# Kernel optimization log

Measured on AMD Instinct MI355X. Metric: run time of the kernel, lower is better.

Reference implementation:

```python
import jax, jax.numpy as jnp
import numpy as np

B, C, H, W = 4, 512, 64, 64


def setup_inputs() -> dict:
    key = jax.random.key(0)
    ks = jax.random.split(key, 9)
    s = 0.02
    return {
        "x": jax.random.normal(ks[0], (B, C, H, W), dtype=jnp.float32),
        "Wq": jax.random.normal(ks[1], (C, C), dtype=jnp.float32) * s,
        "bq": jnp.zeros((C,), dtype=jnp.float32),
        "Wk": jax.random.normal(ks[2], (C, C), dtype=jnp.float32) * s,
        "bk": jnp.zeros((C,), dtype=jnp.float32),
        "Wv": jax.random.normal(ks[3], (C, C), dtype=jnp.float32) * s,
        "bv": jnp.zeros((C,), dtype=jnp.float32),
        "Wo": jax.random.normal(ks[4], (C, C), dtype=jnp.float32) * s,
        "bo": jnp.zeros((C,), dtype=jnp.float32),
    }


def reference(x, Wq, bq, Wk, bk, Wv, bv, Wo, bo):
    b, c, h, w = x.shape
    # (b, c, h, w) -> (b, N, c) flattened spatial tokens
    t = jnp.swapaxes(x.reshape(b, c, h * w), 1, 2)
    q = t @ Wq.T + bq
    k = t @ Wk.T + bk
    v = t @ Wv.T + bv
    scale = 1.0 / jnp.sqrt(jnp.asarray(c, dtype=t.dtype))
    scores = jnp.einsum("bnc,bmc->bnm", q, k) * scale  # (b, N, N)
    attn = jax.nn.softmax(scores, axis=-1)
    out = jnp.einsum("bnm,bmc->bnc", attn, v)
    out = out @ Wo.T + bo  # dropout p=0.0 is identity
    # Faithful to original: direct view (b,N,c) -> (b,c,h,w) WITHOUT permute
    return out.reshape(b, c, h, w)
```

## Files before the change

### kernel.cpp

```cpp
#include <hip/hip_runtime.h>


#define B_ 4
#define C_ 512
#define N_ 4096
#define KV_ 32
#define NSTEP 128

typedef unsigned short u16;
typedef __attribute__((ext_vector_type(8))) short bf16x8;
typedef __attribute__((ext_vector_type(4))) float f32x4;

#define MFMA16(a,b,c) __builtin_amdgcn_mfma_f32_16x16x32_bf16((a),(b),(c),0,0,0)

__device__ inline float exp2_fast(float x){
#if __has_builtin(__builtin_amdgcn_exp2f)
  return __builtin_amdgcn_exp2f(x);
#else
  return exp2f(x);
#endif
}

__device__ inline u16 f2bf(float f){
  unsigned u = __float_as_uint(f);
  u += 0x7FFFu + ((u >> 16) & 1u);
  return (u16)(u >> 16);
}

__device__ __forceinline__ void gload16(const char* g, char* l){
#if __has_builtin(__builtin_amdgcn_global_load_lds)
  __builtin_amdgcn_global_load_lds(
      (const __attribute__((address_space(1))) unsigned int*)(unsigned long long)g,
      (__attribute__((address_space(3))) unsigned int*)(unsigned int)(unsigned long long)l,
      16, 0, 0);
#else
  int lane = threadIdx.x & 63;
  *(uint4*)(l + lane*16) = *(const uint4*)g;
#endif
}

__global__ __launch_bounds__(256) void conv_w_kernel(const float* wq, const float* wk,
                                                     const float* wv, const float* wo, u16* out){
  int i = (blockIdx.x * 256 + threadIdx.x) * 8;
  int mat = i >> 18;
  int within = i & 262143;
  const float* s = (mat==0) ? wq : (mat==1) ? wk : (mat==2) ? wv : wo;
  float4 a = *(const float4*)(s + within);
  float4 b = *(const float4*)(s + within + 4);
  unsigned u0 = f2bf(a.x) | ((unsigned)f2bf(a.y) << 16);
  unsigned u1 = f2bf(a.z) | ((unsigned)f2bf(a.w) << 16);
  unsigned u2 = f2bf(b.x) | ((unsigned)f2bf(b.y) << 16);
  unsigned u3 = f2bf(b.z) | ((unsigned)f2bf(b.w) << 16);
  uint4 v = {u0,u1,u2,u3};
  *(uint4*)(out + i) = v;
}

__global__ __launch_bounds__(256) void transpose_kernel(const float* x, u16* T){
  __shared__ u16 tile[64][66];
  int b = blockIdx.z; int n0 = blockIdx.x*64; int c0 = blockIdx.y*64;
  int t = threadIdx.x;
  const float* xb = x + (size_t)b*C_*N_;
  int nn = t & 63, r0 = t >> 6;
  #pragma unroll
  for (int i=0;i<16;i++){
    int r = r0 + i*4;
    tile[r][nn] = f2bf(xb[(size_t)(c0+r)*N_ + n0 + nn]);
  }
  __syncthreads();
  int nrow = t >> 2, cs = t & 3;
  unsigned u[8];
  #pragma unroll
  for (int j=0;j<8;j++){
    u16 lo = tile[cs*16 + 2*j    ][nrow];
    u16 hi = tile[cs*16 + 2*j + 1][nrow];
    u[j] = lo | ((unsigned)hi << 16);
  }
  u16* dst = T + (size_t)b*N_*C_ + (size_t)(n0+nrow)*C_ + c0 + cs*16;
  uint4 v0 = {u[0],u[1],u[2],u[3]};
  uint4 v1 = {u[4],u[5],u[6],u[7]};
  *(uint4*)(dst)     = v0;
  *(uint4*)(dst + 8) = v1;
}

template<int MODE>
__global__ __launch_bounds__(256) void proj_kernel(const u16* Abase, const u16* Wb,
                                                   const float* b0, const float* b1, const float* b2,
                                                   u16* Qo, u16* Ko, u16* VTo, float* Fo){
  __shared__ char lds[32768];
  char* Al = lds;
  char* Bl = lds + 16384;
  int z = blockIdx.z;
  int b, mat;
  if constexpr (MODE==0){ b = z/3; mat = z - b*3; } else { b = z; mat = 3; }
  const u16* A = Abase + (size_t)b*N_*C_;
  const u16* W = Wb + (size_t)mat*C_*C_;
  const float* bias = (MODE==0) ? (mat==0?b0:(mat==1?b1:b2)) : b0;
  int n0 = blockIdx.x*128, c0 = blockIdx.y*128;
  int t = threadIdx.x, lane = t & 63, w = t >> 6;
  int wm = w >> 1, wn = w & 1;
  int l15 = lane & 15, l4 = lane >> 4;
  f32x4 acc[4][4];
  #pragma unroll
  for (int i=0;i<4;i++)
    #pragma unroll
    for (int j=0;j<4;j++) acc[i][j] = f32x4{0.f,0.f,0.f,0.f};

  for (int ks=0; ks<8; ks++){
    int k0 = ks*64;
    __syncthreads();
    #pragma unroll
    for (int it=0; it<4; it++){
      int idx = it*256 + t, row = idx>>3, ch = idx&7;
      uint4 v = *(const uint4*)(A + (size_t)(n0+row)*C_ + k0 + ch*8);
      *(uint4*)(Al + row*128 + ((ch*16) ^ ((row&7)<<4))) = v;
    }
    #pragma unroll
    for (int it=0; it<4; it++){
      int idx = it*256 + t, row = idx>>3, ch = idx&7;
      uint4 v = *(const uint4*)(W + (size_t)(c0+row)*C_ + k0 + ch*8);
      *(uint4*)(Bl + row*128 + ((ch*16) ^ ((row&7)<<4))) = v;
    }
    __syncthreads();
    #pragma unroll
    for (int kk=0; kk<2; kk++){
      bf16x8 bfrag[4];
      #pragma unroll
      for (int ni=0; ni<4; ni++){
        int br = wn*64 + ni*16 + l15;
        bfrag[ni] = *(const bf16x8*)(Bl + br*128 + ((kk*64 + l4*16) ^ ((br&7)<<4)));
      }
      #pragma unroll
      for (int mi=0; mi<4; mi++){
        int ar = wm*64 + mi*16 + l15;
        bf16x8 afrag = *(const bf16x8*)(Al + ar*128 + ((kk*64 + l4*16) ^ ((ar&7)<<4)));
        #pragma unroll
        for (int ni=0; ni<4; ni++) acc[mi][ni] = MFMA16(afrag, bfrag[ni], acc[mi][ni]);
      }
    }
  }
  #pragma unroll
  for (int mi=0; mi<4; mi++){
    #pragma unroll
    for (int ni=0; ni<4; ni++){
      int col  = c0 + wn*64 + ni*16 + l15;
      int rowb = n0 + wm*64 + mi*16 + l4*4;
      float bb = bias[col];
      if constexpr (MODE==1){
        #pragma unroll
        for (int r=0;r<4;r++)
          Fo[(size_t)b*N_*C_ + (size_t)(rowb+r)*C_ + col] = acc[mi][ni][r] + bb;
      } else {
        if (mat==0){
          #pragma unroll
          for (int r=0;r<4;r++)
            Qo[(size_t)b*N_*C_ + (size_t)(rowb+r)*C_ + col] = f2bf(acc[mi][ni][r] + bb);
        } else if (mat==1){
          #pragma unroll
          for (int r=0;r<4;r++)
            Ko[(size_t)b*N_*C_ + (size_t)(rowb+r)*C_ + col] = f2bf(acc[mi][ni][r] + bb);
        } else {
          ushort4 pk;
          pk.x = f2bf(acc[mi][ni][0] + bb);
          pk.y = f2bf(acc[mi][ni][1] + bb);
          pk.z = f2bf(acc[mi][ni][2] + bb);
          pk.w = f2bf(acc[mi][ni][3] + bb);
          *(ushort4*)(VTo + (size_t)b*(size_t)C_*N_ + (size_t)col*N_ + rowb) = pk;
        }
      }
    }
  }
}

__global__ __launch_bounds__(512) __attribute__((amdgpu_waves_per_eu(2, 2)))
void attn_kernel(const u16* Q, const u16* K, const u16* VT, u16* O){
  extern __shared__ char sm[];
  char* Pl   = sm + 131072;
  float* fac  = (float*)(sm + 135168);
  float* lrow = (float*)(sm + 135424);
  const float SC = (float)(1.4426950408889634 / 22.627416997969522);

  int t = threadIdx.x, lane = t & 63, w = t >> 6;
  int l15 = lane & 15, l4 = lane >> 4;
  int d = blockIdx.x;
  int L = (d & 7)*32 + (d >> 3);
  int b = L >> 6, qt = L & 63;
  int n0 = qt*64;

  const char* Kg = (const char*)K  + (size_t)b*N_*C_*2;
  const char* Vg = (const char*)VT + (size_t)b*C_*N_*2;

  auto stage = [&](int step, int sel){
    int kv0 = step*KV_;
    char* Kn = sm + sel*32768;
    char* Vn = sm + 65536 + sel*32768;
    #pragma unroll
    for (int i=0;i<4;i++){
      int row = w*4 + i;
      gload16(Kg + (size_t)(kv0+row)*1024 + ((lane*16) ^ ((row&7)<<4)), Kn + row*1024);
    }
    int rr = lane >> 2, bb = (lane & 3)*16;
    #pragma unroll
    for (int i=0;i<4;i++){
      int c = w*4 + i;
      gload16(Vg + (size_t)(c*16+rr)*8192 + (size_t)kv0*2 + (bb ^ ((rr&3)<<4)), Vn + c*1024);
    }
  };

  bf16x8 qf[16];
  if (w < 4){
    const u16* qp = Q + ((size_t)b*N_ + n0 + 16*w + l15)*C_ + l4*8;
    #pragma unroll
    for (int kc=0;kc<16;kc++) qf[kc] = *(const bf16x8*)(qp + kc*32);
  }

  f32x4 acc[4][4];
  #pragma unroll
  for (int i=0;i<4;i++)
    #pragma unroll
    for (int j=0;j<4;j++) acc[i][j] = f32x4{0.f,0.f,0.f,0.f};
  float m[4], lsum[4];
  #pragma unroll
  for (int r=0;r<4;r++){ m[r] = -1e30f; lsum[r] = 0.f; }

  stage(0, 0);
  __syncthreads();

  for (int s=0; s<NSTEP; s++){
    char* Kc = sm + (s&1)*32768;
    char* Vc = sm + 65536 + (s&1)*32768;
    if (s+1 < NSTEP) stage(s+1, (s+1)&1);

    if (w < 4){
      f32x4 sa[2];
      sa[0] = f32x4{0.f,0.f,0.f,0.f}; sa[1] = f32x4{0.f,0.f,0.f,0.f};
      #pragma unroll
      for (int kc=0;kc<16;kc++){
        #pragma unroll
        for (int sub=0;sub<2;sub++){
          int kr = sub*16 + l15;
          bf16x8 kf = *(const bf16x8*)(Kc + kr*1024 + ((kc*64 + l4*16) ^ ((kr&7)<<4)));
          sa[sub] = MFMA16(qf[kc], kf, sa[sub]);
        }
      }
      float uu[2][4], pmax[4];
      #pragma unroll
      for (int r=0;r<4;r++){
        float x0 = sa[0][r]*SC, x1 = sa[1][r]*SC;
        uu[0][r]=x0; uu[1][r]=x1;
        pmax[r] = fmaxf(x0,x1);
      }
      #pragma unroll
      for (int off=1; off<16; off<<=1){
        #pragma unroll
        for (int r=0;r<4;r++) pmax[r] = fmaxf(pmax[r], __shfl_xor(pmax[r], off));
      }
      bool need = false;
      #pragma unroll
      for (int r=0;r<4;r++) need = need || (pmax[r] > m[r] + 11.5f);
      float fv[4];
      if (__any(need)){
        #pragma unroll
        for (int r=0;r<4;r++){
          float mn = fmaxf(m[r], pmax[r]);
          fv[r] = exp2_fast(m[r]-mn);
          m[r] = mn; lsum[r] *= fv[r];
        }
      } else {
        #pragma unroll
        for (int r=0;r<4;r++) fv[r] = 1.0f;
      }
      if (l15 == 0){
        #pragma unroll
        for (int r=0;r<4;r++) fac[16*w + l4*4 + r] = fv[r];
      }
      float rs[4] = {0.f,0.f,0.f,0.f};
      #pragma unroll
      for (int sub=0;sub<2;sub++){
        #pragma unroll
        for (int r=0;r<4;r++){
          float p = exp2_fast(uu[sub][r] - m[r]);
          rs[r] += p;
          int row = 16*w + l4*4 + r, col = sub*16 + l15;
          *(u16*)(Pl + row*64 + ((col*2) ^ ((row&3)<<4))) = f2bf(p);
        }
      }
      #pragma unroll
      for (int off=1; off<16; off<<=1){
        #pragma unroll
        for (int r=0;r<4;r++) rs[r] += __shfl_xor(rs[r], off);
      }
      #pragma unroll
      for (int r=0;r<4;r++) lsum[r] += rs[r];
    }
    __syncthreads();

    f32x4 facv[4];
    #pragma unroll
    for (int mi=0;mi<4;mi++) facv[mi] = *(const f32x4*)(fac + mi*16 + l4*4);
    #pragma unroll
    for (int mi=0;mi<4;mi++)
      #pragma unroll
      for (int ni=0;ni<4;ni++)
        #pragma unroll
        for (int r=0;r<4;r++) acc[mi][ni][r] *= facv[mi][r];

    bf16x8 vf[4];
    #pragma unroll
    for (int ni=0;ni<4;ni++){
      int crow = w*64 + ni*16 + l15;
      vf[ni] = *(const bf16x8*)(Vc + crow*64 + ((l4*16) ^ ((crow&3)<<4)));
    }
    #pragma unroll
    for (int mi=0;mi<4;mi++){
      int prow = mi*16 + l15;
      bf16x8 pa = *(const bf16x8*)(Pl + prow*64 + ((l4*16) ^ ((prow&3)<<4)));
      #pragma unroll
      for (int ni=0;ni<4;ni++) acc[mi][ni] = MFMA16(pa, vf[ni], acc[mi][ni]);
    }
    __syncthreads();
  }

  if (w < 4 && l15 == 0){
    #pragma unroll
    for (int r=0;r<4;r++) lrow[16*w + l4*4 + r] = lsum[r];
  }
  __syncthreads();
  u16* Ob = O + ((size_t)b*N_ + n0)*C_;
  #pragma unroll
  for (int mi=0;mi<4;mi++){
    f32x4 lv = *(const f32x4*)(lrow + mi*16 + l4*4);
    f32x4 rl;
    #pragma unroll
    for (int r=0;r<4;r++) rl[r] = 1.0f / lv[r];
    #pragma unroll
    for (int ni=0;ni<4;ni++){
      #pragma unroll
      for (int r=0;r<4;r++){
        int row = mi*16 + l4*4 + r, col = w*64 + ni*16 + l15;
        Ob[(size_t)row*C_ + col] = f2bf(acc[mi][ni][r]*rl[r]);
      }
    }
  }
}

extern "C" void kernel_launch(void* const* d_in, const int* in_sizes, int n_in,
                              void* d_out, int out_size, void* d_ws, size_t ws_size,
                              hipStream_t stream){
  const float* x  = (const float*)d_in[0];
  const float* Wq = (const float*)d_in[1];
  const float* bq = (const float*)d_in[2];
  const float* Wk = (const float*)d_in[3];
  const float* bk = (const float*)d_in[4];
  const float* Wv = (const float*)d_in[5];
  const float* bv = (const float*)d_in[6];
  const float* Wo = (const float*)d_in[7];
  const float* bo = (const float*)d_in[8];

  char* ws = (char*)d_ws;
  u16* Tb  = (u16*)(ws);
  u16* Wbf = (u16*)(ws + 16777216);
  u16* Qw  = (u16*)(ws + 18874368);
  u16* Kw  = (u16*)(ws + 35651584);
  u16* VTw = (u16*)(ws + 52428800);

  hipFuncSetAttribute((const void*)attn_kernel, hipFuncAttributeMaxDynamicSharedMemorySize, 135680);

  conv_w_kernel<<<512,256,0,stream>>>(Wq,Wk,Wv,Wo,Wbf);
  transpose_kernel<<<dim3(64,8,4),256,0,stream>>>(x, Tb);
  proj_kernel<0><<<dim3(32,4,12),256,0,stream>>>(Tb, Wbf, bq,bk,bv, Qw,Kw,VTw,nullptr);
  attn_kernel<<<dim3(256),512,135680,stream>>>(Qw,Kw,VTw,Tb);
  proj_kernel<1><<<dim3(32,4,4),256,0,stream>>>(Tb, Wbf, bo,nullptr,nullptr, nullptr,nullptr,nullptr,(float*)d_out);
}
```

Measured before the change: 444.3 us.

## Split QK^T and softmax across all eight waves with cross-wave max/sum exchange

The score computation and softmax were done by only 4 of the 8 waves while the others idled. Now every wave computes one 16-column half of the KV tile, and the two halves share row maxima and row sums through small LDS buffers. A per-step flag lets waves skip the accumulator rescale when no wave raised its running max. The plain barriers are replaced with explicit waitcnt plus s_barrier helpers, and the P tile swizzle is changed. The cost is an extra barrier per step and a little more LDS, which could hurt if sync latency dominates.

```diff
diff --git a/kernel.cpp b/kernel.cpp
--- a/kernel.cpp
+++ b/kernel.cpp
@@ -25,6 +25,19 @@
   unsigned u = __float_as_uint(f);
   u += 0x7FFFu + ((u >> 16) & 1u);
   return (u16)(u >> 16);
+}
+
+__device__ __forceinline__ void bar_lgkm(){
+  __builtin_amdgcn_sched_barrier(0);
+  asm volatile("s_waitcnt lgkmcnt(0)" ::: "memory");
+  __builtin_amdgcn_s_barrier();
+  __builtin_amdgcn_sched_barrier(0);
+}
+__device__ __forceinline__ void bar_vm(){
+  __builtin_amdgcn_sched_barrier(0);
+  asm volatile("s_waitcnt vmcnt(0) lgkmcnt(0)" ::: "memory");
+  __builtin_amdgcn_s_barrier();
+  __builtin_amdgcn_sched_barrier(0);
 }
 
 __device__ __forceinline__ void gload16(const char* g, char* l){
@@ -174,13 +187,18 @@
 __global__ __launch_bounds__(512) __attribute__((amdgpu_waves_per_eu(2, 2)))
 void attn_kernel(const u16* Q, const u16* K, const u16* VT, u16* O){
   extern __shared__ char sm[];
-  char* Pl   = sm + 131072;
+  char*  Pl   = sm + 131072;
   float* fac  = (float*)(sm + 135168);
   float* lrow = (float*)(sm + 135424);
+  float* pmx  = (float*)(sm + 135680);
+  float* rsx  = (float*)(sm + 136192);
+  int*   flags= (int*)  (sm + 136704);
   const float SC = (float)(1.4426950408889634 / 22.627416997969522);
 
   int t = threadIdx.x, lane = t & 63, w = t >> 6;
   int l15 = lane & 15, l4 = lane >> 4;
+  int g = w & 3;
+  int h = w >> 2;
   int d = blockIdx.x;
   int L = (d & 7)*32 + (d >> 3);
   int b = L >> 6, qt = L & 63;
@@ -207,8 +225,8 @@
   };
 
   bf16x8 qf[16];
-  if (w < 4){
-    const u16* qp = Q + ((size_t)b*N_ + n0 + 16*w + l15)*C_ + l4*8;
+  {
+    const u16* qp = Q + ((size_t)b*N_ + n0 + 16*g + l15)*C_ + l4*8;
     #pragma unroll
     for (int kc=0;kc<16;kc++) qf[kc] = *(const bf16x8*)(qp + kc*32);
   }
@@ -222,87 +240,97 @@
   #pragma unroll
   for (int r=0;r<4;r++){ m[r] = -1e30f; lsum[r] = 0.f; }
 
+  if (t == 0){ flags[0] = 0; flags[1] = 0; }
   stage(0, 0);
-  __syncthreads();
+  bar_vm();
 
   for (int s=0; s<NSTEP; s++){
     char* Kc = sm + (s&1)*32768;
     char* Vc = sm + 65536 + (s&1)*32768;
     if (s+1 < NSTEP) stage(s+1, (s+1)&1);
 
-    if (w < 4){
-      f32x4 sa[2];
-      sa[0] = f32x4{0.f,0.f,0.f,0.f}; sa[1] = f32x4{0.f,0.f,0.f,0.f};
-      #pragma unroll
-      for (int kc=0;kc<16;kc++){
+    f32x4 sa = f32x4{0.f,0.f,0.f,0.f};
+    #pragma unroll
+    for (int kc=0;kc<16;kc++){
+      int kr = h*16 + l15;
+      bf16x8 kf = *(const bf16x8*)(Kc + kr*1024 + ((kc*64 + l4*16) ^ ((kr&7)<<4)));
+      sa = MFMA16(qf[kc], kf, sa);
+    }
+    float x[4], pmax[4];
+    #pragma unroll
+    for (int r=0;r<4;r++){ x[r] = sa[r]*SC; pmax[r] = x[r]; }
+    #pragma unroll
+    for (int off=1; off<16; off<<=1){
+      #pragma unroll
+      for (int r=0;r<4;r++) pmax[r] = fmaxf(pmax[r], __shfl_xor(pmax[r], off));
+    }
+    if (l15 == 0){
+      f32x4 pv = {pmax[0], pmax[1], pmax[2], pmax[3]};
+      *(f32x4*)(pmx + w*16 + l4*4) = pv;
+    }
+    bar_lgkm();
+
+    f32x4 po = *(const f32x4*)(pmx + (w^4)*16 + l4*4);
+    float pm[4];
+    #pragma unroll
+    for (int r=0;r<4;r++) pm[r] = fmaxf(pmax[r], po[r]);
+    bool need = false;
+    #pragma unroll
+    for (int r=0;r<4;r++) need = need || (pm[r] > m[r] + 11.5f);
+    bool wneed = __any(need);
+    float fv[4];
+    if (wneed){
+      #pragma unroll
+      for (int r=0;r<4;r++){
+        float mn = fmaxf(m[r], pm[r]);
+        fv[r] = exp2_fast(m[r]-mn);
+        m[r] = mn; lsum[r] *= fv[r];
+      }
+      if (w < 4 && lane == 0) flags[s&1] = 1;
+    } else {
+      #pragma unroll
+      for (int r=0;r<4;r++) fv[r] = 1.0f;
+    }
+    if (w < 4 && l15 == 0){
+      f32x4 fvv = {fv[0], fv[1], fv[2], fv[3]};
+      *(f32x4*)(fac + g*16 + l4*4) = fvv;
+    }
+    float rs[4];
+    #pragma unroll
+    for (int r=0;r<4;r++){
+      float p = exp2_fast(x[r] - m[r]);
+      rs[r] = p;
+      int row = 16*g + l4*4 + r;
+      *(u16*)(Pl + row*64 + ((((h*16+l15)*2)) ^ (((row>>2)&3)<<4))) = f2bf(p);
+    }
+    #pragma unroll
+    for (int off=1; off<16; off<<=1){
+      #pragma unroll
+      for (int r=0;r<4;r++) rs[r] += __shfl_xor(rs[r], off);
+    }
+    if (l15 == 0){
+      f32x4 rv = {rs[0], rs[1], rs[2], rs[3]};
+      *(f32x4*)(rsx + w*16 + l4*4) = rv;
+    }
+    bar_lgkm();
+
+    f32x4 ro = *(const f32x4*)(rsx + (w^4)*16 + l4*4);
+    #pragma unroll
+    for (int r=0;r<4;r++) lsum[r] += rs[r] + ro[r];
+
+    int fl = flags[s&1];
+    if (t == 0) flags[(s+1)&1] = 0;
+    if (fl){
+      f32x4 facv[4];
+      #pragma unroll
+      for (int mi=0;mi<4;mi++) facv[mi] = *(const f32x4*)(fac + mi*16 + l4*4);
+      #pragma unroll
+      for (int mi=0;mi<4;mi++)
         #pragma unroll
-        for (int sub=0;sub<2;sub++){
-          int kr = sub*16 + l15;
-          bf16x8 kf = *(const bf16x8*)(Kc + kr*1024 + ((kc*64 + l4*16) ^ ((kr&7)<<4)));
-          sa[sub] = MFMA16(qf[kc], kf, sa[sub]);
-        }
-      }
-      float uu[2][4], pmax[4];
-      #pragma unroll
-      for (int r=0;r<4;r++){
-        float x0 = sa[0][r]*SC, x1 = sa[1][r]*SC;
-        uu[0][r]=x0; uu[1][r]=x1;
-        pmax[r] = fmaxf(x0,x1);
-      }
-      #pragma unroll
-      for (int off=1; off<16; off<<=1){
-        #pragma unroll
-        for (int r=0;r<4;r++) pmax[r] = fmaxf(pmax[r], __shfl_xor(pmax[r], off));
-      }
-      bool need = false;
-      #pragma unroll
-      for (int r=0;r<4;r++) need = need || (pmax[r] > m[r] + 11.5f);
-      float fv[4];
-      if (__any(need)){
-        #pragma unroll
-        for (int r=0;r<4;r++){
-          float mn = fmaxf(m[r], pmax[r]);
-          fv[r] = exp2_fast(m[r]-mn);
-          m[r] = mn; lsum[r] *= fv[r];
-        }
-      } else {
-        #pragma unroll
-        for (int r=0;r<4;r++) fv[r] = 1.0f;
-      }
-      if (l15 == 0){
-        #pragma unroll
-        for (int r=0;r<4;r++) fac[16*w + l4*4 + r] = fv[r];
-      }
-      float rs[4] = {0.f,0.f,0.f,0.f};
-      #pragma unroll
-      for (int sub=0;sub<2;sub++){
-        #pragma unroll
-        for (int r=0;r<4;r++){
-          float p = exp2_fast(uu[sub][r] - m[r]);
-          rs[r] += p;
-          int row = 16*w + l4*4 + r, col = sub*16 + l15;
-          *(u16*)(Pl + row*64 + ((col*2) ^ ((row&3)<<4))) = f2bf(p);
-        }
-      }
-      #pragma unroll
-      for (int off=1; off<16; off<<=1){
-        #pragma unroll
-        for (int r=0;r<4;r++) rs[r] += __shfl_xor(rs[r], off);
-      }
-      #pragma unroll
-      for (int r=0;r<4;r++) lsum[r] += rs[r];
-    }
-    __syncthreads();
-
-    f32x4 facv[4];
-    #pragma unroll
-    for (int mi=0;mi<4;mi++) facv[mi] = *(const f32x4*)(fac + mi*16 + l4*4);
-    #pragma unroll
-    for (int mi=0;mi<4;mi++)
-      #pragma unroll
-      for (int ni=0;ni<4;ni++)
-        #pragma unroll
-        for (int r=0;r<4;r++) acc[mi][ni][r] *= facv[mi][r];
+        for (int ni=0;ni<4;ni++)
+          #pragma unroll
+          for (int r=0;r<4;r++) acc[mi][ni][r] *= facv[mi][r];
+    }
 
     bf16x8 vf[4];
     #pragma unroll
@@ -313,18 +341,18 @@
     #pragma unroll
     for (int mi=0;mi<4;mi++){
       int prow = mi*16 + l15;
-      bf16x8 pa = *(const bf16x8*)(Pl + prow*64 + ((l4*16) ^ ((prow&3)<<4)));
+      bf16x8 pa = *(const bf16x8*)(Pl + prow*64 + ((l4*16) ^ (((prow>>2)&3)<<4)));
       #pragma unroll
       for (int ni=0;ni<4;ni++) acc[mi][ni] = MFMA16(pa, vf[ni], acc[mi][ni]);
     }
-    __syncthreads();
+    bar_vm();
   }
 
   if (w < 4 && l15 == 0){
-    #pragma unroll
-    for (int r=0;r<4;r++) lrow[16*w + l4*4 + r] = lsum[r];
-  }
-  __syncthreads();
+    f32x4 lv = {lsum[0], lsum[1], lsum[2], lsum[3]};
+    *(f32x4*)(lrow + g*16 + l4*4) = lv;
+  }
+  bar_lgkm();
   u16* Ob = O + ((size_t)b*N_ + n0)*C_;
   #pragma unroll
   for (int mi=0;mi<4;mi++){
@@ -363,11 +391,11 @@
   u16* Kw  = (u16*)(ws + 35651584);
   u16* VTw = (u16*)(ws + 52428800);
 
-  hipFuncSetAttribute((const void*)attn_kernel, hipFuncAttributeMaxDynamicSharedMemorySize, 135680);
+  hipFuncSetAttribute((const void*)attn_kernel, hipFuncAttributeMaxDynamicSharedMemorySize, 136768);
 
   conv_w_kernel<<<512,256,0,stream>>>(Wq,Wk,Wv,Wo,Wbf);
   transpose_kernel<<<dim3(64,8,4),256,0,stream>>>(x, Tb);
   proj_kernel<0><<<dim3(32,4,12),256,0,stream>>>(Tb, Wbf, bq,bk,bv, Qw,Kw,VTw,nullptr);
-  attn_kernel<<<dim3(256),512,135680,stream>>>(Qw,Kw,VTw,Tb);
+  attn_kernel<<<dim3(256),512,136768,stream>>>(Qw,Kw,VTw,Tb);
   proj_kernel<1><<<dim3(32,4,4),256,0,stream>>>(Tb, Wbf, bo,nullptr,nullptr, nullptr,nullptr,nullptr,(float*)d_out);
 }
```

After: 511.2 us. +15.0%, slower.
